# Optimization experiments

Hardware: AMD Instinct MI355X
Metric: run time of the kernel (lower is better)

## Reference

```python
import jax, jax.numpy as jnp
import numpy as np

N_NODES = 50000
N_EDGES = 800000
NODE_DIM = 10
EDGE_DIM = 5
HID = 64


def _tconv(x, src, dst, e_attr, wq, bq, wk, bk, wv, bv, we, ws, bs):
    # PyG TransformerConv, heads=1, concat=True, root_weight=True, beta=False
    n = x.shape[0]
    q = x @ wq + bq                      # [N, HID]
    k = x @ wk + bk                      # [N, HID]
    v = x @ wv + bv                      # [N, HID]
    ee = e_attr @ we                     # [E, HID] (lin_edge, no bias)
    ke = k[src] + ee                     # key per edge
    ve = v[src] + ee                     # value per edge
    logits = jnp.sum(q[dst] * ke, axis=-1) / 8.0  # sqrt(64) = 8
    m = jax.ops.segment_max(logits, dst, num_segments=n)
    p = jnp.exp(logits - m[dst])
    s = jax.ops.segment_sum(p, dst, num_segments=n)
    alpha = p / s[dst]                   # segment softmax over in-neighbors
    agg = jax.ops.segment_sum(alpha[:, None] * ve, dst, num_segments=n)
    return agg + x @ ws + bs             # + lin_skip(x_i)


def setup_inputs() -> dict:
    key = jax.random.key(0)
    ks = jax.random.split(key, 32)
    x = jax.random.uniform(ks[0], (N_NODES, NODE_DIM), dtype=jnp.float32)
    edge_index = jax.random.randint(ks[1], (2, N_EDGES), 0, N_NODES, dtype=jnp.int64)
    edge_attr = jax.random.uniform(ks[2], (N_EDGES, EDGE_DIM), dtype=jnp.float32)

    def lin(k, fan_in, fan_out):
        b = 1.0 / np.sqrt(fan_in)
        return jax.random.uniform(k, (fan_in, fan_out), jnp.float32, -b, b)

    def bias(k, fan_in, fan_out):
        b = 1.0 / np.sqrt(fan_in)
        return jax.random.uniform(k, (fan_out,), jnp.float32, -b, b)

    inp = dict(x=x, edge_index=edge_index, edge_attr=edge_attr)
    # conv1: NODE_DIM -> HID
    inp['w1q'] = lin(ks[3], NODE_DIM, HID); inp['b1q'] = bias(ks[4], NODE_DIM, HID)
    inp['w1k'] = lin(ks[5], NODE_DIM, HID); inp['b1k'] = bias(ks[6], NODE_DIM, HID)
    inp['w1v'] = lin(ks[7], NODE_DIM, HID); inp['b1v'] = bias(ks[8], NODE_DIM, HID)
    inp['w1e'] = lin(ks[9], EDGE_DIM, HID)
    inp['w1s'] = lin(ks[10], NODE_DIM, HID); inp['b1s'] = bias(ks[11], NODE_DIM, HID)
    # 5 stacked HID -> HID layers
    inp['wq'] = jnp.stack([lin(jax.random.fold_in(ks[12], i), HID, HID) for i in range(5)])
    inp['bq'] = jnp.stack([bias(jax.random.fold_in(ks[13], i), HID, HID) for i in range(5)])
    inp['wk'] = jnp.stack([lin(jax.random.fold_in(ks[14], i), HID, HID) for i in range(5)])
    inp['bk'] = jnp.stack([bias(jax.random.fold_in(ks[15], i), HID, HID) for i in range(5)])
    inp['wv'] = jnp.stack([lin(jax.random.fold_in(ks[16], i), HID, HID) for i in range(5)])
    inp['bv'] = jnp.stack([bias(jax.random.fold_in(ks[17], i), HID, HID) for i in range(5)])
    inp['we'] = jnp.stack([lin(jax.random.fold_in(ks[18], i), EDGE_DIM, HID) for i in range(5)])
    inp['ws'] = jnp.stack([lin(jax.random.fold_in(ks[19], i), HID, HID) for i in range(5)])
    inp['bs'] = jnp.stack([bias(jax.random.fold_in(ks[20], i), HID, HID) for i in range(5)])
    # final linear HID -> 1
    inp['lin_w'] = lin(ks[21], HID, 1); inp['lin_b'] = bias(ks[22], HID, 1)
    return inp


def reference(x, edge_index, edge_attr, w1q, b1q, w1k, b1k, w1v, b1v, w1e, w1s, b1s,
              wq, bq, wk, bk, wv, bv, we, ws, bs, lin_w, lin_b):
    src, dst = edge_index[0], edge_index[1]  # x_j = x[src], aggregated into dst
    h = jnp.log(x + 1.0)
    e = jnp.log(edge_attr + 1.0)
    h = _tconv(h, src, dst, e, w1q, b1q, w1k, b1k, w1v, b1v, w1e, w1s, b1s)
    for i in range(5):
        h = _tconv(h, src, dst, e, wq[i], bq[i], wk[i], bk[i], wv[i], bv[i], we[i], ws[i], bs[i])
    return h @ lin_w + lin_b  # [N, 1]
```

## Files before the change

kernel.cpp:

```cpp
#include <hip/hip_runtime.h>
#include <cstdint>
#include <cstddef>

#define NN 50000
#define NE 800000
#define HD 64
#define SB 49

__global__ void k_hist(const int* __restrict__ ei, int* __restrict__ cnt) {
    int e = blockIdx.x * blockDim.x + threadIdx.x;
    if (e < NE) atomicAdd(&cnt[ei[NE + e]], 1);
}

__global__ __launch_bounds__(256) void k_scan1(const int* __restrict__ cnt,
                                               int* __restrict__ row_start,
                                               int* __restrict__ bsum) {
    __shared__ int ssum[256];
    const int tid = threadIdx.x, b = blockIdx.x;
    const int i0 = b * 1024 + tid * 4;
    int c0 = 0, c1 = 0, c2 = 0, c3 = 0;
    if (i0 + 3 < NN) {
        const int4 c = *(const int4*)(cnt + i0);
        c0 = c.x; c1 = c.y; c2 = c.z; c3 = c.w;
    } else {
        if (i0 + 0 < NN) c0 = cnt[i0 + 0];
        if (i0 + 1 < NN) c1 = cnt[i0 + 1];
        if (i0 + 2 < NN) c2 = cnt[i0 + 2];
        if (i0 + 3 < NN) c3 = cnt[i0 + 3];
    }
    ssum[tid] = c0 + c1 + c2 + c3;
    __syncthreads();
    for (int off = 1; off < 256; off <<= 1) {
        int v = (tid >= off) ? ssum[tid - off] : 0;
        __syncthreads();
        ssum[tid] += v;
        __syncthreads();
    }
    int ex = (tid == 0) ? 0 : ssum[tid - 1];
    if (i0 + 0 < NN) row_start[i0 + 0] = ex;
    ex += c0;
    if (i0 + 1 < NN) row_start[i0 + 1] = ex;
    ex += c1;
    if (i0 + 2 < NN) row_start[i0 + 2] = ex;
    ex += c2;
    if (i0 + 3 < NN) row_start[i0 + 3] = ex;
    if (tid == 255) bsum[b] = ssum[255];
}

__global__ __launch_bounds__(64) void k_scan2(const int* __restrict__ bsum,
                                              int* __restrict__ boff,
                                              int* __restrict__ row_start) {
    __shared__ int s[64];
    const int t = threadIdx.x;
    s[t] = (t < SB) ? bsum[t] : 0;
    __syncthreads();
    for (int off = 1; off < 64; off <<= 1) {
        int v = (t >= off) ? s[t - off] : 0;
        __syncthreads();
        s[t] += v;
        __syncthreads();
    }
    if (t < SB) boff[t] = (t == 0) ? 0 : s[t - 1];
    if (t == 0) row_start[NN] = s[SB - 1];
}

__global__ __launch_bounds__(256) void k_scan3(int* __restrict__ row_start,
                                               const int* __restrict__ boff,
                                               int* __restrict__ cur) {
    const int b = blockIdx.x;
    const int i0 = b * 1024 + threadIdx.x * 4;
    const int o = boff[b];
#pragma unroll
    for (int k = 0; k < 4; ++k) {
        int i = i0 + k;
        if (i < NN) {
            int v = row_start[i] + o;
            row_start[i] = v;
            cur[i] = v;
        }
    }
}

__global__ void k_scatter(const int* __restrict__ ei, const float* __restrict__ ea,
                          int* __restrict__ cur, float* __restrict__ e5s) {
    int e = blockIdx.x * blockDim.x + threadIdx.x;
    if (e < NE) {
        int d = ei[NE + e];
        int pos = atomicAdd(&cur[d], 1);
        float4 lo;
        lo.x = __logf(ea[e * 5 + 0] + 1.f);
        lo.y = __logf(ea[e * 5 + 1] + 1.f);
        lo.z = __logf(ea[e * 5 + 2] + 1.f);
        lo.w = __logf(ea[e * 5 + 3] + 1.f);
        float4 hi;
        hi.x = __logf(ea[e * 5 + 4] + 1.f);
        hi.y = __int_as_float(ei[e] << 9);
        hi.z = 0.f;
        hi.w = 0.f;
        *(float4*)(e5s + (size_t)pos * 8) = lo;
        *(float4*)(e5s + (size_t)pos * 8 + 4) = hi;
    }
}

__global__ __launch_bounds__(256) void k_qkvs64(
    const float* __restrict__ h,
    const float* __restrict__ Wq, const float* __restrict__ Bq,
    const float* __restrict__ Wk, const float* __restrict__ Bk,
    const float* __restrict__ Wv, const float* __restrict__ Bv,
    const float* __restrict__ Ws, const float* __restrict__ Bs,
    float* __restrict__ qb, float* __restrict__ kvb, float* __restrict__ sb) {
    __shared__ float xs[4][256];
    const int lane = threadIdx.x & 63;
    const int w = threadIdx.x >> 6;
    const int pair = w >> 1, half = w & 1;
    const float* W0 = half ? Wv : Wq;
    const float* B0 = half ? Bv : Bq;
    const float* W1 = half ? Ws : Wk;
    const float* B1 = half ? Bs : Bk;
    float* O0 = half ? (kvb + 64) : qb;
    float* O1 = half ? sb : kvb;
    const int ldo0 = half ? 128 : 64;
    const int ldo1 = half ? 64 : 128;
    const float scl0 = half ? 1.f : 0.125f;
    float w0[64], w1[64];
#pragma unroll
    for (int j = 0; j < 64; ++j) {
        w0[j] = W0[j * 64 + lane] * scl0;
        w1[j] = W1[j * 64 + lane];
    }
    const float b0 = B0[lane] * scl0, b1 = B1[lane];
    const int nquad = NN / 4;
    const int step = gridDim.x * 2;
    int quad = blockIdx.x * 2 + pair;
    if (quad >= nquad) return;
    {
        const float4 g = *(const float4*)(h + (size_t)quad * 256 + lane * 4);
        *(float4*)&xs[w][lane * 4] = g;
    }
    while (true) {
        const int nq = quad + step;
        const bool more = nq < nquad;
        float4 gn;
        if (more) gn = *(const float4*)(h + (size_t)nq * 256 + lane * 4);
        float a0[4] = {b0, b0, b0, b0};
        float a1[4] = {b1, b1, b1, b1};
#pragma unroll
        for (int jq = 0; jq < 16; ++jq) {
#pragma unroll
            for (int n = 0; n < 4; ++n) {
                const float4 xv = *(const float4*)&xs[w][n * 64 + jq * 4];
                a0[n] = fmaf(xv.x, w0[jq * 4 + 0], a0[n]);
                a1[n] = fmaf(xv.x, w1[jq * 4 + 0], a1[n]);
                a0[n] = fmaf(xv.y, w0[jq * 4 + 1], a0[n]);
                a1[n] = fmaf(xv.y, w1[jq * 4 + 1], a1[n]);
                a0[n] = fmaf(xv.z, w0[jq * 4 + 2], a0[n]);
                a1[n] = fmaf(xv.z, w1[jq * 4 + 2], a1[n]);
                a0[n] = fmaf(xv.w, w0[jq * 4 + 3], a0[n]);
                a1[n] = fmaf(xv.w, w1[jq * 4 + 3], a1[n]);
            }
        }
#pragma unroll
        for (int n = 0; n < 4; ++n) {
            O0[(size_t)(quad * 4 + n) * ldo0 + lane] = a0[n];
            O1[(size_t)(quad * 4 + n) * ldo1 + lane] = a1[n];
        }
        if (!more) break;
        *(float4*)&xs[w][lane * 4] = gn;
        quad = nq;
    }
}

__global__ __launch_bounds__(256, 4) void k_qkvs10(
    const float* __restrict__ x,
    const float* __restrict__ Wq, const float* __restrict__ Bq,
    const float* __restrict__ Wk, const float* __restrict__ Bk,
    const float* __restrict__ Wv, const float* __restrict__ Bv,
    const float* __restrict__ Ws, const float* __restrict__ Bs,
    float* __restrict__ qb, float* __restrict__ kvb, float* __restrict__ sb) {
    __shared__ float xs[640];
    const int lane = threadIdx.x & 63;
    const int w = threadIdx.x >> 6;
    const float* W = (w == 0) ? Wq : (w == 1) ? Wk : (w == 2) ? Wv : Ws;
    const float* B = (w == 0) ? Bq : (w == 1) ? Bk : (w == 2) ? Bv : Bs;
    float* outp = (w == 0) ? qb : (w == 1) ? kvb : (w == 2) ? (kvb + 64) : sb;
    const int ldo = (w == 1 || w == 2) ? 128 : 64;
    const float scl = (w == 0) ? 0.125f : 1.f;
    float wr[10];
#pragma unroll
    for (int j = 0; j < 10; ++j) wr[j] = W[j * 64 + lane] * scl;
    const float bias = B[lane] * scl;
    const int tile = blockIdx.x;
    const int fbase = tile * 640;
    const int fcnt = min(640, NN * 10 - fbase);
    if (threadIdx.x * 4 < fcnt) {
        float4 v = *(const float4*)(x + (size_t)fbase + threadIdx.x * 4);
        v.x = __logf(v.x + 1.f);
        v.y = __logf(v.y + 1.f);
        v.z = __logf(v.z + 1.f);
        v.w = __logf(v.w + 1.f);
        *(float4*)&xs[threadIdx.x * 4] = v;
    }
    __syncthreads();
    const int nbase = tile * 64;
    const int nodes = min(64, NN - nbase);
    for (int n = 0; n < nodes; ++n) {
        float acc = bias;
#pragma unroll
        for (int j = 0; j < 10; ++j) acc = fmaf(xs[n * 10 + j], wr[j], acc);
        outp[(size_t)(nbase + n) * ldo + lane] = acc;
    }
}

template <bool FINAL>
__global__ __launch_bounds__(256) void k_agg(
    const float* __restrict__ q, const float* __restrict__ kv,
    const float* __restrict__ sk, const float* __restrict__ e5s,
    const float* __restrict__ wE, const int* __restrict__ row_start,
    float* __restrict__ hout, const float* __restrict__ lw, const float* lb) {
    const int lane = threadIdx.x & 63;
    const int g = lane >> 4, t = lane & 15;
    const int node = __builtin_amdgcn_readfirstlane(blockIdx.x * 4 + (threadIdx.x >> 6));
    if (node >= NN) return;
    const int beg = row_start[node], end = row_start[node + 1];
    if (beg == end) {
        const float4 s4 = *(const float4*)(sk + (size_t)node * 64 + t * 4);
        if (FINAL) {
            const float4 lw4 = *(const float4*)(lw + t * 4);
            float r = s4.x * lw4.x;
            r = fmaf(s4.y, lw4.y, r);
            r = fmaf(s4.z, lw4.z, r);
            r = fmaf(s4.w, lw4.w, r);
            r += __shfl_xor(r, 1);
            r += __shfl_xor(r, 2);
            r += __shfl_xor(r, 4);
            r += __shfl_xor(r, 8);
            if (lane == 0) hout[node] = r + lb[0];
        } else if (g == 0) {
            *(float4*)(hout + (size_t)node * 64 + t * 4) = s4;
        }
        return;
    }
    const float4 q4 = *(const float4*)(q + (size_t)node * 64 + t * 4);
    float g5[5];
    {
        const float4 wg = *(const float4*)(wE + g * 64 + t * 4);
        float dc = q4.x * wg.x;
        dc = fmaf(q4.y, wg.y, dc);
        dc = fmaf(q4.z, wg.z, dc);
        dc = fmaf(q4.w, wg.w, dc);
        dc += __shfl_xor(dc, 1);
        dc += __shfl_xor(dc, 2);
        dc += __shfl_xor(dc, 4);
        dc += __shfl_xor(dc, 8);
        const float4 w4 = *(const float4*)(wE + 4 * 64 + t * 4);
        float d4 = q4.x * w4.x;
        d4 = fmaf(q4.y, w4.y, d4);
        d4 = fmaf(q4.z, w4.z, d4);
        d4 = fmaf(q4.w, w4.w, d4);
        d4 += __shfl_xor(d4, 1);
        d4 += __shfl_xor(d4, 2);
        d4 += __shfl_xor(d4, 4);
        d4 += __shfl_xor(d4, 8);
        g5[0] = __shfl(dc, 0);
        g5[1] = __shfl(dc, 16);
        g5[2] = __shfl(dc, 32);
        g5[3] = __shfl(dc, 48);
        g5[4] = __shfl(d4, 0);
    }
    float m = -1e30f, l = 0.f;
    float4 accv = {0.f, 0.f, 0.f, 0.f};
    float a50 = 0.f, a51 = 0.f, a52 = 0.f, a53 = 0.f, a54 = 0.f;
    const char* kvc = (const char*)kv;
    const int i0x = beg + g;
    const int i0 = (i0x < end) ? i0x : beg;
    float4 e0lo = *(const float4*)(e5s + (size_t)i0 * 8);
    float2 e0hi = *(const float2*)(e5s + (size_t)i0 * 8 + 4);
    const int i1x = beg + 4 + g;
    const int i1 = (i1x < end) ? i1x : beg;
    float4 e1lo = *(const float4*)(e5s + (size_t)i1 * 8);
    float2 e1hi = *(const float2*)(e5s + (size_t)i1 * 8 + 4);
    const float* kp0 = (const float*)(kvc + (size_t)(unsigned)__float_as_int(e0hi.y)) + t * 4;
    float4 k4 = *(const float4*)(kp0);
    float4 v4 = *(const float4*)(kp0 + 64);
#pragma unroll 2
    for (int p = beg; p < end; p += 4) {
        const int nx = p + 8 + g;
        const int npp = (nx < end) ? nx : beg;
        const float4 nlo = *(const float4*)(e5s + (size_t)npp * 8);
        const float2 nhi = *(const float2*)(e5s + (size_t)npp * 8 + 4);
        const float* kpn =
            (const float*)(kvc + (size_t)(unsigned)__float_as_int(e1hi.y)) + t * 4;
        const float4 nk4 = *(const float4*)(kpn);
        const float4 nv4 = *(const float4*)(kpn + 64);
        const bool act = (p + g) < end;
        float d = q4.x * k4.x;
        d = fmaf(q4.y, k4.y, d);
        d = fmaf(q4.z, k4.z, d);
        d = fmaf(q4.w, k4.w, d);
        d += __shfl_xor(d, 1);
        d += __shfl_xor(d, 2);
        d += __shfl_xor(d, 4);
        d += __shfl_xor(d, 8);
        float d5 = g5[0] * e0lo.x;
        d5 = fmaf(g5[1], e0lo.y, d5);
        d5 = fmaf(g5[2], e0lo.z, d5);
        d5 = fmaf(g5[3], e0lo.w, d5);
        d5 = fmaf(g5[4], e0hi.x, d5);
        const float la = act ? (d + d5) : -1e30f;
        const float nm = fmaxf(m, la);
        const float scl = __expf(m - nm);
        const float pa = __expf(la - nm);
        l = fmaf(l, scl, pa);
        accv.x = fmaf(accv.x, scl, pa * v4.x);
        accv.y = fmaf(accv.y, scl, pa * v4.y);
        accv.z = fmaf(accv.z, scl, pa * v4.z);
        accv.w = fmaf(accv.w, scl, pa * v4.w);
        a50 = fmaf(a50, scl, pa * e0lo.x);
        a51 = fmaf(a51, scl, pa * e0lo.y);
        a52 = fmaf(a52, scl, pa * e0lo.z);
        a53 = fmaf(a53, scl, pa * e0lo.w);
        a54 = fmaf(a54, scl, pa * e0hi.x);
        m = nm;
        e0lo = e1lo;
        e0hi = e1hi;
        e1lo = nlo;
        e1hi = nhi;
        k4 = nk4;
        v4 = nv4;
    }
    float M = fmaxf(m, __shfl_xor(m, 16));
    M = fmaxf(M, __shfl_xor(M, 32));
    const float f = __expf(m - M);
    float lz = l * f;
    lz += __shfl_xor(lz, 16);
    lz += __shfl_xor(lz, 32);
    accv.x *= f;
    accv.y *= f;
    accv.z *= f;
    accv.w *= f;
    a50 *= f;
    a51 *= f;
    a52 *= f;
    a53 *= f;
    a54 *= f;
#pragma unroll
    for (int s = 16; s <= 32; s <<= 1) {
        accv.x += __shfl_xor(accv.x, s);
        accv.y += __shfl_xor(accv.y, s);
        accv.z += __shfl_xor(accv.z, s);
        accv.w += __shfl_xor(accv.w, s);
        a50 += __shfl_xor(a50, s);
        a51 += __shfl_xor(a51, s);
        a52 += __shfl_xor(a52, s);
        a53 += __shfl_xor(a53, s);
        a54 += __shfl_xor(a54, s);
    }
    float4 t4 = accv;
    {
        const float4 w0 = *(const float4*)(wE + 0 * 64 + t * 4);
        const float4 w1 = *(const float4*)(wE + 1 * 64 + t * 4);
        const float4 w2 = *(const float4*)(wE + 2 * 64 + t * 4);
        const float4 w3 = *(const float4*)(wE + 3 * 64 + t * 4);
        const float4 w4r = *(const float4*)(wE + 4 * 64 + t * 4);
        t4.x = fmaf(a50, w0.x, t4.x);
        t4.y = fmaf(a50, w0.y, t4.y);
        t4.z = fmaf(a50, w0.z, t4.z);
        t4.w = fmaf(a50, w0.w, t4.w);
        t4.x = fmaf(a51, w1.x, t4.x);
        t4.y = fmaf(a51, w1.y, t4.y);
        t4.z = fmaf(a51, w1.z, t4.z);
        t4.w = fmaf(a51, w1.w, t4.w);
        t4.x = fmaf(a52, w2.x, t4.x);
        t4.y = fmaf(a52, w2.y, t4.y);
        t4.z = fmaf(a52, w2.z, t4.z);
        t4.w = fmaf(a52, w2.w, t4.w);
        t4.x = fmaf(a53, w3.x, t4.x);
        t4.y = fmaf(a53, w3.y, t4.y);
        t4.z = fmaf(a53, w3.z, t4.z);
        t4.w = fmaf(a53, w3.w, t4.w);
        t4.x = fmaf(a54, w4r.x, t4.x);
        t4.y = fmaf(a54, w4r.y, t4.y);
        t4.z = fmaf(a54, w4r.z, t4.z);
        t4.w = fmaf(a54, w4r.w, t4.w);
    }
    const float4 s4 = *(const float4*)(sk + (size_t)node * 64 + t * 4);
    const float rl = 1.f / lz;
    float4 o;
    o.x = fmaf(t4.x, rl, s4.x);
    o.y = fmaf(t4.y, rl, s4.y);
    o.z = fmaf(t4.z, rl, s4.z);
    o.w = fmaf(t4.w, rl, s4.w);
    if (FINAL) {
        const float4 lw4 = *(const float4*)(lw + t * 4);
        float r = o.x * lw4.x;
        r = fmaf(o.y, lw4.y, r);
        r = fmaf(o.z, lw4.z, r);
        r = fmaf(o.w, lw4.w, r);
        r += __shfl_xor(r, 1);
        r += __shfl_xor(r, 2);
        r += __shfl_xor(r, 4);
        r += __shfl_xor(r, 8);
        if (lane == 0) hout[node] = r + lb[0];
    } else if (g == 0) {
        *(float4*)(hout + (size_t)node * 64 + t * 4) = o;
    }
}

extern "C" void kernel_launch(void* const* d_in, const int* in_sizes, int n_in,
                              void* d_out, int out_size, void* d_ws, size_t ws_size,
                              hipStream_t stream) {
    const float* x = (const float*)d_in[0];
    const int* ei = (const int*)d_in[1];
    const float* ea = (const float*)d_in[2];
    const float* w1q = (const float*)d_in[3];
    const float* b1q = (const float*)d_in[4];
    const float* w1k = (const float*)d_in[5];
    const float* b1k = (const float*)d_in[6];
    const float* w1v = (const float*)d_in[7];
    const float* b1v = (const float*)d_in[8];
    const float* w1e = (const float*)d_in[9];
    const float* w1s = (const float*)d_in[10];
    const float* b1s = (const float*)d_in[11];
    const float* wq = (const float*)d_in[12];
    const float* bq = (const float*)d_in[13];
    const float* wk = (const float*)d_in[14];
    const float* bk = (const float*)d_in[15];
    const float* wv = (const float*)d_in[16];
    const float* bv = (const float*)d_in[17];
    const float* we = (const float*)d_in[18];
    const float* ws = (const float*)d_in[19];
    const float* bs = (const float*)d_in[20];
    const float* lw = (const float*)d_in[21];
    const float* lb = (const float*)d_in[22];

    uintptr_t p = (uintptr_t)d_ws;
    auto alloc = [&](size_t bytes) -> void* {
        void* r = (void*)p;
        p += (bytes + 255) & ~(size_t)255;
        return r;
    };
    float* e5s = (float*)alloc((size_t)NE * 8 * 4);
    float* hb = (float*)alloc((size_t)NN * HD * 4);
    float* kvb = (float*)alloc((size_t)NN * 128 * 4);
    float* qb = (float*)alloc((size_t)NN * HD * 4);
    float* sb = (float*)alloc((size_t)NN * HD * 4);
    int* row_start = (int*)alloc((size_t)(NN + 1) * 4);
    int* cnt = (int*)alloc((size_t)NN * 4);
    int* cur = (int*)alloc((size_t)NN * 4);
    int* bsum = (int*)alloc((size_t)SB * 4);
    int* boff = (int*)alloc((size_t)SB * 4);

    hipMemsetAsync(cnt, 0, (size_t)NN * 4, stream);
    k_hist<<<(NE + 255) / 256, 256, 0, stream>>>(ei, cnt);
    k_scan1<<<SB, 256, 0, stream>>>(cnt, row_start, bsum);
    k_scan2<<<1, 64, 0, stream>>>(bsum, boff, row_start);
    k_scan3<<<SB, 256, 0, stream>>>(row_start, boff, cur);
    k_scatter<<<(NE + 255) / 256, 256, 0, stream>>>(ei, ea, cur, e5s);

    const int gg64 = 768;
    const int gg10 = (NN + 63) / 64;
    const int agg_grid = (NN + 3) / 4;

    k_qkvs10<<<gg10, 256, 0, stream>>>(x, w1q, b1q, w1k, b1k, w1v, b1v, w1s, b1s,
                                       qb, kvb, sb);
    k_agg<false><<<agg_grid, 256, 0, stream>>>(qb, kvb, sb, e5s, w1e, row_start, hb,
                                               lw, lb);

    for (int i = 0; i < 5; ++i) {
        k_qkvs64<<<gg64, 256, 0, stream>>>(hb, wq + i * 4096, bq + i * 64,
                                           wk + i * 4096, bk + i * 64,
                                           wv + i * 4096, bv + i * 64,
                                           ws + i * 4096, bs + i * 64,
                                           qb, kvb, sb);
        if (i < 4) {
            k_agg<false><<<agg_grid, 256, 0, stream>>>(qb, kvb, sb, e5s, we + i * 320,
                                                       row_start, hb, lw, lb);
        } else {
            k_agg<true><<<agg_grid, 256, 0, stream>>>(qb, kvb, sb, e5s, we + i * 320,
                                                      row_start, (float*)d_out, lw, lb);
        }
    }
}
```

Measured before the change: 719.5 us.

## Store K/V in fp16 interleaved layout and split edge records into packed arrays

The projection kernels now write K and V as half precision, interleaved per 4-element group, so each edge gather in the aggregation kernel reads one 16-byte load instead of two 16-byte float loads. The edge records are split into a float4 attribute array and a float2 array holding the fifth attribute and the source byte offset, cutting padding from 32 to 24 bytes per edge. This lowers gather and streaming bandwidth in the dominant aggregation kernel. In exchange, K and V lose precision, which compounds across six layers, and the projection kernels now issue scattered 2-byte stores.

Measured after the change: 783.3 us. 8.9% more time.

```diff
diff --git a/kernel.cpp b/kernel.cpp
--- a/kernel.cpp
+++ b/kernel.cpp
@@ -1,4 +1,5 @@
 #include <hip/hip_runtime.h>
+#include <hip/hip_fp16.h>
 #include <cstdint>
 #include <cstddef>
 
@@ -82,7 +83,8 @@
 }
 
 __global__ void k_scatter(const int* __restrict__ ei, const float* __restrict__ ea,
-                          int* __restrict__ cur, float* __restrict__ e5s) {
+                          int* __restrict__ cur, float* __restrict__ e5lo,
+                          float* __restrict__ e5hi) {
     int e = blockIdx.x * blockDim.x + threadIdx.x;
     if (e < NE) {
         int d = ei[NE + e];
@@ -92,14 +94,23 @@
         lo.y = __logf(ea[e * 5 + 1] + 1.f);
         lo.z = __logf(ea[e * 5 + 2] + 1.f);
         lo.w = __logf(ea[e * 5 + 3] + 1.f);
-        float4 hi;
+        float2 hi;
         hi.x = __logf(ea[e * 5 + 4] + 1.f);
-        hi.y = __int_as_float(ei[e] << 9);
-        hi.z = 0.f;
-        hi.w = 0.f;
-        *(float4*)(e5s + (size_t)pos * 8) = lo;
-        *(float4*)(e5s + (size_t)pos * 8 + 4) = hi;
-    }
+        hi.y = __int_as_float(ei[e] << 8);
+        *(float4*)(e5lo + (size_t)pos * 4) = lo;
+        *(float2*)(e5hi + (size_t)pos * 2) = hi;
+    }
+}
+
+__device__ __forceinline__ float4 cvt_k(const uint4 u) {
+    const float2 a = __half22float2(*(const __half2*)&u.x);
+    const float2 b = __half22float2(*(const __half2*)&u.y);
+    return make_float4(a.x, a.y, b.x, b.y);
+}
+__device__ __forceinline__ float4 cvt_v(const uint4 u) {
+    const float2 a = __half22float2(*(const __half2*)&u.z);
+    const float2 b = __half22float2(*(const __half2*)&u.w);
+    return make_float4(a.x, a.y, b.x, b.y);
 }
 
 __global__ __launch_bounds__(256) void k_qkvs64(
@@ -108,7 +119,7 @@
     const float* __restrict__ Wk, const float* __restrict__ Bk,
     const float* __restrict__ Wv, const float* __restrict__ Bv,
     const float* __restrict__ Ws, const float* __restrict__ Bs,
-    float* __restrict__ qb, float* __restrict__ kvb, float* __restrict__ sb) {
+    float* __restrict__ qb, __half* __restrict__ kvh, float* __restrict__ sb) {
     __shared__ float xs[4][256];
     const int lane = threadIdx.x & 63;
     const int w = threadIdx.x >> 6;
@@ -117,11 +128,8 @@
     const float* B0 = half ? Bv : Bq;
     const float* W1 = half ? Ws : Wk;
     const float* B1 = half ? Bs : Bk;
-    float* O0 = half ? (kvb + 64) : qb;
-    float* O1 = half ? sb : kvb;
-    const int ldo0 = half ? 128 : 64;
-    const int ldo1 = half ? 64 : 128;
     const float scl0 = half ? 1.f : 0.125f;
+    const int koff = ((lane >> 2) << 3) + (lane & 3);
     float w0[64], w1[64];
 #pragma unroll
     for (int j = 0; j < 64; ++j) {
@@ -161,8 +169,14 @@
         }
 #pragma unroll
         for (int n = 0; n < 4; ++n) {
-            O0[(size_t)(quad * 4 + n) * ldo0 + lane] = a0[n];
-            O1[(size_t)(quad * 4 + n) * ldo1 + lane] = a1[n];
+            const size_t node = (size_t)(quad * 4 + n);
+            if (half == 0) {
+                qb[node * 64 + lane] = a0[n];
+                kvh[node * 128 + koff] = __float2half(a1[n]);
+            } else {
+                kvh[node * 128 + koff + 4] = __float2half(a0[n]);
+                sb[node * 64 + lane] = a1[n];
+            }
         }
         if (!more) break;
         *(float4*)&xs[w][lane * 4] = gn;
@@ -176,15 +190,15 @@
     const float* __restrict__ Wk, const float* __restrict__ Bk,
     const float* __restrict__ Wv, const float* __restrict__ Bv,
     const float* __restrict__ Ws, const float* __restrict__ Bs,
-    float* __restrict__ qb, float* __restrict__ kvb, float* __restrict__ sb) {
+    float* __restrict__ qb, __half* __restrict__ kvh, float* __restrict__ sb) {
     __shared__ float xs[640];
     const int lane = threadIdx.x & 63;
     const int w = threadIdx.x >> 6;
     const float* W = (w == 0) ? Wq : (w == 1) ? Wk : (w == 2) ? Wv : Ws;
     const float* B = (w == 0) ? Bq : (w == 1) ? Bk : (w == 2) ? Bv : Bs;
-    float* outp = (w == 0) ? qb : (w == 1) ? kvb : (w == 2) ? (kvb + 64) : sb;
-    const int ldo = (w == 1 || w == 2) ? 128 : 64;
+    float* outp = (w == 0) ? qb : sb;
     const float scl = (w == 0) ? 0.125f : 1.f;
+    const int koff = ((lane >> 2) << 3) + (lane & 3);
     float wr[10];
 #pragma unroll
     for (int j = 0; j < 10; ++j) wr[j] = W[j * 64 + lane] * scl;
@@ -207,16 +221,20 @@
         float acc = bias;
 #pragma unroll
         for (int j = 0; j < 10; ++j) acc = fmaf(xs[n * 10 + j], wr[j], acc);
-        outp[(size_t)(nbase + n) * ldo + lane] = acc;
+        const size_t node = (size_t)(nbase + n);
+        if (w == 1) kvh[node * 128 + koff] = __float2half(acc);
+        else if (w == 2) kvh[node * 128 + koff + 4] = __float2half(acc);
+        else outp[node * 64 + lane] = acc;
     }
 }
 
 template <bool FINAL>
 __global__ __launch_bounds__(256) void k_agg(
-    const float* __restrict__ q, const float* __restrict__ kv,
-    const float* __restrict__ sk, const float* __restrict__ e5s,
-    const float* __restrict__ wE, const int* __restrict__ row_start,
-    float* __restrict__ hout, const float* __restrict__ lw, const float* lb) {
+    const float* __restrict__ q, const __half* __restrict__ kv,
+    const float* __restrict__ sk, const float* __restrict__ e5lo,
+    const float* __restrict__ e5hi, const float* __restrict__ wE,
+    const int* __restrict__ row_start, float* __restrict__ hout,
+    const float* __restrict__ lw, const float* lb) {
     const int lane = threadIdx.x & 63;
     const int g = lane >> 4, t = lane & 15;
     const int node = __builtin_amdgcn_readfirstlane(blockIdx.x * 4 + (threadIdx.x >> 6));
@@ -273,26 +291,24 @@
     const char* kvc = (const char*)kv;
     const int i0x = beg + g;
     const int i0 = (i0x < end) ? i0x : beg;
-    float4 e0lo = *(const float4*)(e5s + (size_t)i0 * 8);
-    float2 e0hi = *(const float2*)(e5s + (size_t)i0 * 8 + 4);
+    float4 e0lo = *(const float4*)(e5lo + (size_t)i0 * 4);
+    float2 e0hi = *(const float2*)(e5hi + (size_t)i0 * 2);
     const int i1x = beg + 4 + g;
     const int i1 = (i1x < end) ? i1x : beg;
-    float4 e1lo = *(const float4*)(e5s + (size_t)i1 * 8);
-    float2 e1hi = *(const float2*)(e5s + (size_t)i1 * 8 + 4);
-    const float* kp0 = (const float*)(kvc + (size_t)(unsigned)__float_as_int(e0hi.y)) + t * 4;
-    float4 k4 = *(const float4*)(kp0);
-    float4 v4 = *(const float4*)(kp0 + 64);
+    float4 e1lo = *(const float4*)(e5lo + (size_t)i1 * 4);
+    float2 e1hi = *(const float2*)(e5hi + (size_t)i1 * 2);
+    uint4 kv8 = *(const uint4*)(kvc + (size_t)(unsigned)__float_as_int(e0hi.y) + t * 16);
 #pragma unroll 2
     for (int p = beg; p < end; p += 4) {
         const int nx = p + 8 + g;
         const int npp = (nx < end) ? nx : beg;
-        const float4 nlo = *(const float4*)(e5s + (size_t)npp * 8);
-        const float2 nhi = *(const float2*)(e5s + (size_t)npp * 8 + 4);
-        const float* kpn =
-            (const float*)(kvc + (size_t)(unsigned)__float_as_int(e1hi.y)) + t * 4;
-        const float4 nk4 = *(const float4*)(kpn);
-        const float4 nv4 = *(const float4*)(kpn + 64);
+        const float4 nlo = *(const float4*)(e5lo + (size_t)npp * 4);
+        const float2 nhi = *(const float2*)(e5hi + (size_t)npp * 2);
+        const uint4 nkv =
+            *(const uint4*)(kvc + (size_t)(unsigned)__float_as_int(e1hi.y) + t * 16);
         const bool act = (p + g) < end;
+        const float4 k4 = cvt_k(kv8);
+        const float4 v4 = cvt_v(kv8);
         float d = q4.x * k4.x;
         d = fmaf(q4.y, k4.y, d);
         d = fmaf(q4.z, k4.z, d);
@@ -325,8 +341,7 @@
         e0hi = e1hi;
         e1lo = nlo;
         e1hi = nhi;
-        k4 = nk4;
-        v4 = nv4;
+        kv8 = nkv;
     }
     float M = fmaxf(m, __shfl_xor(m, 16));
     M = fmaxf(M, __shfl_xor(M, 32));
@@ -439,9 +454,10 @@
         p += (bytes + 255) & ~(size_t)255;
         return r;
     };
-    float* e5s = (float*)alloc((size_t)NE * 8 * 4);
+    float* e5lo = (float*)alloc((size_t)NE * 4 * 4);
+    float* e5hi = (float*)alloc((size_t)NE * 2 * 4);
     float* hb = (float*)alloc((size_t)NN * HD * 4);
-    float* kvb = (float*)alloc((size_t)NN * 128 * 4);
+    __half* kvh = (__half*)alloc((size_t)NN * 128 * 2);
     float* qb = (float*)alloc((size_t)NN * HD * 4);
     float* sb = (float*)alloc((size_t)NN * HD * 4);
     int* row_start = (int*)alloc((size_t)(NN + 1) * 4);
@@ -455,29 +471,31 @@
     k_scan1<<<SB, 256, 0, stream>>>(cnt, row_start, bsum);
     k_scan2<<<1, 64, 0, stream>>>(bsum, boff, row_start);
     k_scan3<<<SB, 256, 0, stream>>>(row_start, boff, cur);
-    k_scatter<<<(NE + 255) / 256, 256, 0, stream>>>(ei, ea, cur, e5s);
+    k_scatter<<<(NE + 255) / 256, 256, 0, stream>>>(ei, ea, cur, e5lo, e5hi);
 
     const int gg64 = 768;
     const int gg10 = (NN + 63) / 64;
     const int agg_grid = (NN + 3) / 4;
 
     k_qkvs10<<<gg10, 256, 0, stream>>>(x, w1q, b1q, w1k, b1k, w1v, b1v, w1s, b1s,
-                                       qb, kvb, sb);
-    k_agg<false><<<agg_grid, 256, 0, stream>>>(qb, kvb, sb, e5s, w1e, row_start, hb,
-                                               lw, lb);
+                                       qb, kvh, sb);
+    k_agg<false><<<agg_grid, 256, 0, stream>>>(qb, kvh, sb, e5lo, e5hi, w1e,
+                                               row_start, hb, lw, lb);
 
     for (int i = 0; i < 5; ++i) {
         k_qkvs64<<<gg64, 256, 0, stream>>>(hb, wq + i * 4096, bq + i * 64,
                                            wk + i * 4096, bk + i * 64,
                                            wv + i * 4096, bv + i * 64,
                                            ws + i * 4096, bs + i * 64,
-                                           qb, kvb, sb);
+                                           qb, kvh, sb);
         if (i < 4) {
-            k_agg<false><<<agg_grid, 256, 0, stream>>>(qb, kvb, sb, e5s, we + i * 320,
-                                                       row_start, hb, lw, lb);
+            k_agg<false><<<agg_grid, 256, 0, stream>>>(qb, kvh, sb, e5lo, e5hi,
+                                                       we + i * 320, row_start, hb,
+                                                       lw, lb);
         } else {
-            k_agg<true><<<agg_grid, 256, 0, stream>>>(qb, kvb, sb, e5s, we + i * 320,
-                                                      row_start, (float*)d_out, lw, lb);
+            k_agg<true><<<agg_grid, 256, 0, stream>>>(qb, kvh, sb, e5lo, e5hi,
+                                                      we + i * 320, row_start,
+                                                      (float*)d_out, lw, lb);
         }
     }
 }
```
